# Kernel optimization log

Hardware: AMD Instinct MI355X
Metric: run time of the kernel (lower is better)

Reference implementation:

```python
import jax, jax.numpy as jnp
import numpy as np

B, L, D = 32, 2048, 1024


def setup_inputs() -> dict:
    key = jax.random.key(0)
    ks = jax.random.split(key, 8)
    s = 1.0 / np.sqrt(D).astype(np.float32)  # torch nn.Linear init scale
    return {
        "decoder_hidden": jax.random.normal(ks[0], (B, 1, D), jnp.float32),
        "encoder_outputs": jax.random.normal(ks[1], (B, L, D), jnp.float32),
        "W_w": jax.random.uniform(ks[2], (D, D), jnp.float32, -s, s),
        "W_b": jax.random.uniform(ks[3], (D,), jnp.float32, -s, s),
        "U_w": jax.random.uniform(ks[4], (D, D), jnp.float32, -s, s),
        "U_b": jax.random.uniform(ks[5], (D,), jnp.float32, -s, s),
        "v_w": jax.random.uniform(ks[6], (1, D), jnp.float32, -s, s),
        "v_b": jax.random.uniform(ks[7], (1,), jnp.float32, -s, s),
    }


def reference(decoder_hidden, encoder_outputs, W_w, W_b, U_w, U_b, v_w, v_b):
    # torch Linear: y = x @ W.T + b
    q = decoder_hidden @ W_w.T + W_b            # [B, 1, D]
    k = encoder_outputs @ U_w.T + U_b           # [B, L, D]
    scores = jnp.tanh(q + k) @ v_w.T + v_b      # [B, L, 1]
    attn = jax.nn.softmax(scores[..., 0], axis=-1)[:, None, :]  # [B, 1, L]
    context = jnp.einsum("bql,bld->bqd", attn, encoder_outputs)  # [B, 1, D]
    return (context, attn)
```

## Files before the change

kernel.cpp:

```cpp
#include <hip/hip_runtime.h>
#include <hip/hip_bf16.h>
#include <stdint.h>

#define BB 32
#define LL 2048
#define DD 1024

typedef short short8 __attribute__((ext_vector_type(8)));
typedef float f32x4  __attribute__((ext_vector_type(4)));

__device__ __forceinline__ short f2bf(float f) {
    unsigned u = __float_as_uint(f);
    u += 0x7fffu + ((u >> 16) & 1u);
    return (short)(u >> 16);
}

__device__ __forceinline__ float fast_tanh(float x) {
    float e = __expf(2.f * x);
    return 1.f - 2.f * __builtin_amdgcn_rcpf(e + 1.f);
}

__device__ __forceinline__ void async_cp16(const void* g, void* l) {
    __builtin_amdgcn_global_load_lds(
        (__attribute__((address_space(1))) void*)g,
        (__attribute__((address_space(3))) void*)l, 16, 0, 0);
}

__global__ void cvt_bf16_kernel(const float* __restrict__ src, short* __restrict__ dst) {
    int idx = (blockIdx.x * 256 + threadIdx.x) * 8;
    float4 a = *(const float4*)(src + idx);
    float4 c = *(const float4*)(src + idx + 4);
    short8 p;
    p[0] = f2bf(a.x); p[1] = f2bf(a.y); p[2] = f2bf(a.z); p[3] = f2bf(a.w);
    p[4] = f2bf(c.x); p[5] = f2bf(c.y); p[6] = f2bf(c.z); p[7] = f2bf(c.w);
    *(short8*)(dst + idx) = p;
}

__global__ void q_kernel(const float* __restrict__ dh, const float* __restrict__ Ww,
                         const float* __restrict__ Wb, const float* __restrict__ Ub,
                         float* __restrict__ qbuf) {
    int b  = blockIdx.x >> 4;
    int d0 = (blockIdx.x & 15) << 6;
    int t = threadIdx.x, w = t >> 6, lane = t & 63;
    __shared__ __align__(16) float hs[DD];
    *(float4*)&hs[t * 4] = *(const float4*)&dh[b * DD + t * 4];
    __syncthreads();
    float hr[16];
#pragma unroll
    for (int i = 0; i < 16; i++) hr[i] = hs[lane + 64 * i];
    for (int i = 0; i < 16; i++) {
        int d = d0 + w * 16 + i;
        const float* wr = Ww + (size_t)d * DD;
        float s = 0.f;
#pragma unroll
        for (int j = 0; j < 16; j++) s += wr[lane + 64 * j] * hr[j];
#pragma unroll
        for (int m = 1; m < 64; m <<= 1) s += __shfl_xor(s, m, 64);
        if (lane == 0) qbuf[b * DD + d] = s + Wb[d] + Ub[d];
    }
}

__global__ __launch_bounds__(256, 3) void gemm_scores_bf(
    const short* __restrict__ encbf, const short* __restrict__ Ubf,
    const float* __restrict__ qbuf, const float* __restrict__ vw,
    float* __restrict__ spart) {
    __shared__ __align__(16) short As[128 * 32];
    __shared__ __align__(16) short Bs[128 * 32];
    __shared__ float q_s[128], v_s[128], s_acc[2][128];

    const int t = threadIdx.x;
    const int lane = t & 63, w = t >> 6;
    const int l15 = lane & 15, quad = lane >> 4;
    const int wm = w >> 1, wn = w & 1;
    const int n0 = blockIdx.x << 7;
    const int m0 = blockIdx.y << 7;
    const int b  = m0 >> 11;

    if (t < 128) {
        q_s[t] = qbuf[(b << 10) + n0 + t];
        v_s[t] = vw[n0 + t];
    }

    f32x4 acc[4][4];
#pragma unroll
    for (int i = 0; i < 4; i++)
#pragma unroll
        for (int j = 0; j < 4; j++) acc[i][j] = (f32x4){0.f, 0.f, 0.f, 0.f};

    const int srow = lane >> 2, sseg = (lane & 3) << 3;
    const short* gA0 = encbf + (((size_t)(m0 + w * 32 + srow)) << 10) + sseg;
    const short* gB0 = Ubf   + (((size_t)(n0 + w * 32 + srow)) << 10) + sseg;
    short* lA0 = As + w * 32 * 32;
    short* lB0 = Bs + w * 32 * 32;

    for (int k0 = 0; k0 < 1024; k0 += 32) {
        __syncthreads();
        async_cp16(gA0 + k0, lA0);
        async_cp16(gA0 + k0 + (16 << 10), lA0 + 16 * 32);
        async_cp16(gB0 + k0, lB0);
        async_cp16(gB0 + k0 + (16 << 10), lB0 + 16 * 32);
        __syncthreads();

        short8 af[4], bfv[4];
#pragma unroll
        for (int mt = 0; mt < 4; mt++)
            af[mt] = *(const short8*)&As[(wm * 64 + mt * 16 + l15) * 32 + quad * 8];
#pragma unroll
        for (int nt = 0; nt < 4; nt++)
            bfv[nt] = *(const short8*)&Bs[(wn * 64 + nt * 16 + l15) * 32 + quad * 8];
#pragma unroll
        for (int mt = 0; mt < 4; mt++)
#pragma unroll
            for (int nt = 0; nt < 4; nt++)
                acc[mt][nt] = __builtin_amdgcn_mfma_f32_16x16x32_bf16(
                    af[mt], bfv[nt], acc[mt][nt], 0, 0, 0);
    }

    float qn[4], vn[4];
#pragma unroll
    for (int nt = 0; nt < 4; nt++) {
        qn[nt] = q_s[wn * 64 + nt * 16 + l15];
        vn[nt] = v_s[wn * 64 + nt * 16 + l15];
    }
#pragma unroll
    for (int mt = 0; mt < 4; mt++) {
#pragma unroll
        for (int r = 0; r < 4; r++) {
            float sum = 0.f;
#pragma unroll
            for (int nt = 0; nt < 4; nt++)
                sum += vn[nt] * fast_tanh(acc[mt][nt][r] + qn[nt]);
            sum += __shfl_xor(sum, 1, 64);
            sum += __shfl_xor(sum, 2, 64);
            sum += __shfl_xor(sum, 4, 64);
            sum += __shfl_xor(sum, 8, 64);
            if (l15 == 0)
                s_acc[wn][wm * 64 + mt * 16 + quad * 4 + r] = sum;
        }
    }
    __syncthreads();
    if (t < 128)
        spart[((size_t)blockIdx.x << 16) + m0 + t] = s_acc[0][t] + s_acc[1][t];
}

__global__ __launch_bounds__(256, 3) void gemm_scores_f32(
    const float* __restrict__ enc, const short* __restrict__ Ubf,
    const float* __restrict__ qbuf, const float* __restrict__ vw,
    float* __restrict__ scores) {
    __shared__ __align__(16) short As[128 * 32];
    __shared__ __align__(16) short Bs[128 * 32];
    __shared__ float q_s[128], v_s[128], s_acc[128];

    const int t = threadIdx.x;
    const int lane = t & 63, w = t >> 6;
    const int l15 = lane & 15, quad = lane >> 4;
    const int wm = w >> 1, wn = w & 1;
    const int n0 = blockIdx.x << 7;
    const int m0 = blockIdx.y << 7;
    const int b  = m0 >> 11;

    if (t < 128) {
        q_s[t] = qbuf[(b << 10) + n0 + t];
        v_s[t] = vw[n0 + t];
        s_acc[t] = 0.f;
    }

    f32x4 acc[4][4];
#pragma unroll
    for (int i = 0; i < 4; i++)
#pragma unroll
        for (int j = 0; j < 4; j++) acc[i][j] = (f32x4){0.f, 0.f, 0.f, 0.f};

    const int arow = t >> 1, ahalf = t & 1;
    const float* aptr = enc + (((size_t)(m0 + arow)) << 10) + (ahalf << 4);
    short* adst = As + arow * 32 + ahalf * 16;
    const int brow = t >> 2, bks = (t & 3) * 8;
    const short* bptr1 = Ubf + ((size_t)(n0 + brow)) * 1024 + bks;
    const short* bptr2 = bptr1 + (size_t)64 * 1024;
    short* bdst1 = Bs + brow * 32 + bks;
    short* bdst2 = bdst1 + 64 * 32;

    for (int k0 = 0; k0 < 1024; k0 += 32) {
        __syncthreads();
        float4 f0 = *(const float4*)(aptr + k0);
        float4 f1 = *(const float4*)(aptr + k0 + 4);
        float4 f2 = *(const float4*)(aptr + k0 + 8);
        float4 f3 = *(const float4*)(aptr + k0 + 12);
        short8 p0, p1;
        p0[0] = f2bf(f0.x); p0[1] = f2bf(f0.y); p0[2] = f2bf(f0.z); p0[3] = f2bf(f0.w);
        p0[4] = f2bf(f1.x); p0[5] = f2bf(f1.y); p0[6] = f2bf(f1.z); p0[7] = f2bf(f1.w);
        p1[0] = f2bf(f2.x); p1[1] = f2bf(f2.y); p1[2] = f2bf(f2.z); p1[3] = f2bf(f2.w);
        p1[4] = f2bf(f3.x); p1[5] = f2bf(f3.y); p1[6] = f2bf(f3.z); p1[7] = f2bf(f3.w);
        *(short8*)adst = p0;
        *(short8*)(adst + 8) = p1;
        *(short8*)bdst1 = *(const short8*)(bptr1 + k0);
        *(short8*)bdst2 = *(const short8*)(bptr2 + k0);
        __syncthreads();

        short8 af[4], bfv[4];
#pragma unroll
        for (int mt = 0; mt < 4; mt++)
            af[mt] = *(const short8*)&As[(wm * 64 + mt * 16 + l15) * 32 + quad * 8];
#pragma unroll
        for (int nt = 0; nt < 4; nt++)
            bfv[nt] = *(const short8*)&Bs[(wn * 64 + nt * 16 + l15) * 32 + quad * 8];
#pragma unroll
        for (int mt = 0; mt < 4; mt++)
#pragma unroll
            for (int nt = 0; nt < 4; nt++)
                acc[mt][nt] = __builtin_amdgcn_mfma_f32_16x16x32_bf16(
                    af[mt], bfv[nt], acc[mt][nt], 0, 0, 0);
    }

    float qn[4], vn[4];
#pragma unroll
    for (int nt = 0; nt < 4; nt++) {
        qn[nt] = q_s[wn * 64 + nt * 16 + l15];
        vn[nt] = v_s[wn * 64 + nt * 16 + l15];
    }
#pragma unroll
    for (int mt = 0; mt < 4; mt++) {
#pragma unroll
        for (int r = 0; r < 4; r++) {
            float sum = 0.f;
#pragma unroll
            for (int nt = 0; nt < 4; nt++)
                sum += vn[nt] * fast_tanh(acc[mt][nt][r] + qn[nt]);
            sum += __shfl_xor(sum, 1, 64);
            sum += __shfl_xor(sum, 2, 64);
            sum += __shfl_xor(sum, 4, 64);
            sum += __shfl_xor(sum, 8, 64);
            if (l15 == 0)
                atomicAdd(&s_acc[wm * 64 + mt * 16 + quad * 4 + r], sum);
        }
    }
    __syncthreads();
    if (t < 128) atomicAdd(&scores[m0 + t], s_acc[t]);
}

__global__ void softmax_kernel(const float* __restrict__ sp, int npart,
                               float* __restrict__ attn) {
    int b = blockIdx.x, t = threadIdx.x;
    int w = t >> 6, lane = t & 63;
    __shared__ float rm[4], rs[4];
    float v[8];
#pragma unroll
    for (int i = 0; i < 8; i++) {
        float s = 0.f;
        for (int p = 0; p < npart; p++) s += sp[p * 65536 + (b << 11) + t + (i << 8)];
        v[i] = s;
    }
    float m = v[0];
#pragma unroll
    for (int i = 1; i < 8; i++) m = fmaxf(m, v[i]);
#pragma unroll
    for (int s = 1; s < 64; s <<= 1) m = fmaxf(m, __shfl_xor(m, s, 64));
    if (lane == 0) rm[w] = m;
    __syncthreads();
    m = fmaxf(fmaxf(rm[0], rm[1]), fmaxf(rm[2], rm[3]));
    float s = 0.f;
#pragma unroll
    for (int i = 0; i < 8; i++) { v[i] = __expf(v[i] - m); s += v[i]; }
#pragma unroll
    for (int k = 1; k < 64; k <<= 1) s += __shfl_xor(s, k, 64);
    if (lane == 0) rs[w] = s;
    __syncthreads();
    s = rs[0] + rs[1] + rs[2] + rs[3];
    float inv = 1.f / s;
#pragma unroll
    for (int i = 0; i < 8; i++) attn[(b << 11) + t + (i << 8)] = v[i] * inv;
}

__global__ void context_kernel(const float* __restrict__ enc, const float* __restrict__ attn,
                               float* __restrict__ ctx) {
    int dchunk = blockIdx.x, b = blockIdx.y;
    int t = threadIdx.x;
    __shared__ __align__(16) float at_s[2048];
    __shared__ float red[16][128];
    *(float4*)&at_s[t * 4] = *(const float4*)&attn[(b << 11) + t * 4];
    __syncthreads();
    int d4 = (t & 31) << 2;
    int dl = t >> 5;
    int d0 = dchunk << 7;
    const float* base = enc + ((size_t)b << 21) + d0 + d4;
    float ax = 0.f, ay = 0.f, az = 0.f, aw = 0.f;
#pragma unroll 4
    for (int i = 0; i < 128; i++) {
        int l = (i << 4) + dl;
        float wg = at_s[l];
        float4 e = *(const float4*)(base + ((size_t)l << 10));
        ax += wg * e.x; ay += wg * e.y; az += wg * e.z; aw += wg * e.w;
    }
    red[dl][d4 + 0] = ax;
    red[dl][d4 + 1] = ay;
    red[dl][d4 + 2] = az;
    red[dl][d4 + 3] = aw;
    __syncthreads();
    if (t < 128) {
        float s = 0.f;
#pragma unroll
        for (int j = 0; j < 16; j++) s += red[j][t];
        ctx[(b << 10) + d0 + t] = s;
    }
}

extern "C" void kernel_launch(void* const* d_in, const int* in_sizes, int n_in,
                              void* d_out, int out_size, void* d_ws, size_t ws_size,
                              hipStream_t stream) {
    const float* dh  = (const float*)d_in[0];
    const float* enc = (const float*)d_in[1];
    const float* Ww  = (const float*)d_in[2];
    const float* Wb  = (const float*)d_in[3];
    const float* Uw  = (const float*)d_in[4];
    const float* Ub  = (const float*)d_in[5];
    const float* vw  = (const float*)d_in[6];

    float* out  = (float*)d_out;
    float* attn = out + BB * DD;
    char*  ws   = (char*)d_ws;
    short* Ubf   = (short*)ws;
    float* qbuf  = (float*)(ws + (2 << 20));
    float* sbuf  = (float*)(ws + (2 << 20) + (1 << 17));
    short* encbf = (short*)(ws + (8 << 20));

    bool bigws = ws_size >= ((size_t)143 << 20);

    cvt_bf16_kernel<<<512, 256, 0, stream>>>(Uw, Ubf);
    q_kernel<<<512, 256, 0, stream>>>(dh, Ww, Wb, Ub, qbuf);

    if (bigws) {
        cvt_bf16_kernel<<<32768, 256, 0, stream>>>(enc, encbf);
        gemm_scores_bf<<<dim3(8, 512), 256, 0, stream>>>(encbf, Ubf, qbuf, vw, sbuf);
        softmax_kernel<<<BB, 256, 0, stream>>>(sbuf, 8, attn);
    } else {
        hipMemsetAsync(sbuf, 0, (size_t)BB * LL * sizeof(float), stream);
        gemm_scores_f32<<<dim3(8, 512), 256, 0, stream>>>(enc, Ubf, qbuf, vw, sbuf);
        softmax_kernel<<<BB, 256, 0, stream>>>(sbuf, 1, attn);
    }
    context_kernel<<<dim3(8, BB), 512, 0, stream>>>(enc, attn, out);
}
```

Before: 637.7 us.

## Fuse softmax into bf16 context kernel and remap GEMM blocks per XCD

Replaces the separate softmax and fp32 context kernels on the large-workspace path with one kernel. Each block reduces the partial scores, computes the softmax, and does the weighted sum over the bf16 copy of the encoder outputs, so the context pass reads half the bytes. The scores GEMM also remaps block indices so each XCD works on a contiguous set of M stripes, with all 8 N blocks of a stripe in consecutive slots, to improve L2 reuse of the encoder tile. In exchange, each of the 8 blocks per batch repeats the softmax, and the context now uses bf16-rounded encoder values.

Result: faster. 592.9 us (-7.0%).

```diff
diff --git a/kernel.cpp b/kernel.cpp
--- a/kernel.cpp
+++ b/kernel.cpp
@@ -6,13 +6,17 @@
 #define LL 2048
 #define DD 1024
 
-typedef short short8 __attribute__((ext_vector_type(8)));
-typedef float f32x4  __attribute__((ext_vector_type(4)));
+typedef short short8  __attribute__((ext_vector_type(8)));
+typedef float f32x4   __attribute__((ext_vector_type(4)));
 
 __device__ __forceinline__ short f2bf(float f) {
     unsigned u = __float_as_uint(f);
     u += 0x7fffu + ((u >> 16) & 1u);
     return (short)(u >> 16);
+}
+
+__device__ __forceinline__ float bf2f(unsigned short s) {
+    return __uint_as_float(((unsigned)s) << 16);
 }
 
 __device__ __forceinline__ float fast_tanh(float x) {
@@ -72,8 +76,14 @@
     const int lane = t & 63, w = t >> 6;
     const int l15 = lane & 15, quad = lane >> 4;
     const int wm = w >> 1, wn = w & 1;
-    const int n0 = blockIdx.x << 7;
-    const int m0 = blockIdx.y << 7;
+
+    const int lin  = blockIdx.x + (blockIdx.y << 3);
+    const int xcd  = lin & 7;
+    const int slot = lin >> 3;
+    const int nblk = slot & 7;
+    const int mstripe = (xcd << 6) + (slot >> 3);
+    const int n0 = nblk << 7;
+    const int m0 = mstripe << 7;
     const int b  = m0 >> 11;
 
     if (t < 128) {
@@ -140,7 +150,79 @@
     }
     __syncthreads();
     if (t < 128)
-        spart[((size_t)blockIdx.x << 16) + m0 + t] = s_acc[0][t] + s_acc[1][t];
+        spart[((size_t)nblk << 16) + m0 + t] = s_acc[0][t] + s_acc[1][t];
+}
+
+__global__ void ctx_softmax_bf(const float* __restrict__ sp, const short* __restrict__ encbf,
+                               float* __restrict__ attn, float* __restrict__ ctx) {
+    const int dchunk = blockIdx.x, b = blockIdx.y;
+    const int t = threadIdx.x;
+    const int w = t >> 6, lane = t & 63;
+    __shared__ float at_s[2048];
+    __shared__ float red[16][128];
+    __shared__ float rr[8];
+
+    float v[4];
+#pragma unroll
+    for (int i = 0; i < 4; i++) {
+        int l = t + (i << 9);
+        float s = 0.f;
+#pragma unroll
+        for (int p = 0; p < 8; p++) s += sp[(p << 16) + (b << 11) + l];
+        v[i] = s;
+    }
+    float m = fmaxf(fmaxf(v[0], v[1]), fmaxf(v[2], v[3]));
+#pragma unroll
+    for (int s = 1; s < 64; s <<= 1) m = fmaxf(m, __shfl_xor(m, s, 64));
+    if (lane == 0) rr[w] = m;
+    __syncthreads();
+    m = rr[0];
+#pragma unroll
+    for (int i = 1; i < 8; i++) m = fmaxf(m, rr[i]);
+    float s = 0.f;
+#pragma unroll
+    for (int i = 0; i < 4; i++) { v[i] = __expf(v[i] - m); s += v[i]; }
+#pragma unroll
+    for (int k = 1; k < 64; k <<= 1) s += __shfl_xor(s, k, 64);
+    __syncthreads();
+    if (lane == 0) rr[w] = s;
+#pragma unroll
+    for (int i = 0; i < 4; i++) at_s[t + (i << 9)] = v[i];
+    __syncthreads();
+    s = 0.f;
+#pragma unroll
+    for (int i = 0; i < 8; i++) s += rr[i];
+    float inv = 1.f / s;
+
+    if (dchunk == 0) {
+#pragma unroll
+        for (int i = 0; i < 4; i++) attn[(b << 11) + t + (i << 9)] = v[i] * inv;
+    }
+
+    const int d4 = (t & 31) << 2;
+    const int dl = t >> 5;
+    const int d0 = dchunk << 7;
+    const short* base = encbf + ((size_t)b << 21) + d0 + d4;
+    float ax = 0.f, ay = 0.f, az = 0.f, aw = 0.f;
+#pragma unroll 4
+    for (int i = 0; i < 128; i++) {
+        int l = (i << 4) + dl;
+        float wg = at_s[l];
+        ushort4 e = *(const ushort4*)(base + ((size_t)l << 10));
+        ax += wg * bf2f(e.x); ay += wg * bf2f(e.y);
+        az += wg * bf2f(e.z); aw += wg * bf2f(e.w);
+    }
+    red[dl][d4 + 0] = ax;
+    red[dl][d4 + 1] = ay;
+    red[dl][d4 + 2] = az;
+    red[dl][d4 + 3] = aw;
+    __syncthreads();
+    if (t < 128) {
+        float acc = 0.f;
+#pragma unroll
+        for (int j = 0; j < 16; j++) acc += red[j][t];
+        ctx[(b << 10) + d0 + t] = acc * inv;
+    }
 }
 
 __global__ __launch_bounds__(256, 3) void gemm_scores_f32(
@@ -238,18 +320,13 @@
     if (t < 128) atomicAdd(&scores[m0 + t], s_acc[t]);
 }
 
-__global__ void softmax_kernel(const float* __restrict__ sp, int npart,
-                               float* __restrict__ attn) {
+__global__ void softmax_kernel(const float* __restrict__ sp, float* __restrict__ attn) {
     int b = blockIdx.x, t = threadIdx.x;
     int w = t >> 6, lane = t & 63;
     __shared__ float rm[4], rs[4];
     float v[8];
 #pragma unroll
-    for (int i = 0; i < 8; i++) {
-        float s = 0.f;
-        for (int p = 0; p < npart; p++) s += sp[p * 65536 + (b << 11) + t + (i << 8)];
-        v[i] = s;
-    }
+    for (int i = 0; i < 8; i++) v[i] = sp[(b << 11) + t + (i << 8)];
     float m = v[0];
 #pragma unroll
     for (int i = 1; i < 8; i++) m = fmaxf(m, v[i]);
@@ -271,8 +348,8 @@
     for (int i = 0; i < 8; i++) attn[(b << 11) + t + (i << 8)] = v[i] * inv;
 }
 
-__global__ void context_kernel(const float* __restrict__ enc, const float* __restrict__ attn,
-                               float* __restrict__ ctx) {
+__global__ void context_f32(const float* __restrict__ enc, const float* __restrict__ attn,
+                            float* __restrict__ ctx) {
     int dchunk = blockIdx.x, b = blockIdx.y;
     int t = threadIdx.x;
     __shared__ __align__(16) float at_s[2048];
@@ -331,11 +408,11 @@
     if (bigws) {
         cvt_bf16_kernel<<<32768, 256, 0, stream>>>(enc, encbf);
         gemm_scores_bf<<<dim3(8, 512), 256, 0, stream>>>(encbf, Ubf, qbuf, vw, sbuf);
-        softmax_kernel<<<BB, 256, 0, stream>>>(sbuf, 8, attn);
+        ctx_softmax_bf<<<dim3(8, BB), 512, 0, stream>>>(sbuf, encbf, attn, out);
     } else {
         hipMemsetAsync(sbuf, 0, (size_t)BB * LL * sizeof(float), stream);
         gemm_scores_f32<<<dim3(8, 512), 256, 0, stream>>>(enc, Ubf, qbuf, vw, sbuf);
-        softmax_kernel<<<BB, 256, 0, stream>>>(sbuf, 1, attn);
-    }
-    context_kernel<<<dim3(8, BB), 512, 0, stream>>>(enc, attn, out);
-}
+        softmax_kernel<<<BB, 256, 0, stream>>>(sbuf, attn);
+        context_f32<<<dim3(8, BB), 512, 0, stream>>>(enc, attn, out);
+    }
+}
```
